# Kernel tuning notes

Measured on AMD Instinct MI355X. Metric: run time of the kernel, lower is better.

The kernel has to match this reference:

```python
import jax, jax.numpy as jnp
import numpy as np
import math

B_SZ = 2
SEQ = 4000
D_MODEL = 768
D_INNER = 1536
D_STATE = 16
D_CONV = 4
DT_RANK = 48
NSLICES = 5


def setup_inputs() -> dict:
    key = jax.random.key(0)
    ks = jax.random.split(key, 9)
    s = 0.02
    hidden_states = jax.random.normal(ks[0], (B_SZ, SEQ, D_MODEL), jnp.float32)
    in_proj_w = jax.random.normal(ks[1], (2 * D_INNER, D_MODEL), jnp.float32) * s
    conv_w = jax.random.normal(ks[2], (3, D_INNER, 1, D_CONV), jnp.float32) * 0.3
    x_proj_w = jax.random.normal(ks[3], (3, DT_RANK + 2 * D_STATE, D_INNER), jnp.float32) * s
    dt_proj_w = jax.random.uniform(ks[4], (3, D_INNER, DT_RANK), jnp.float32,
                                   -(DT_RANK ** -0.5), DT_RANK ** -0.5)
    # dt bias: inverse-softplus of dt ~ LogUniform(1e-3, 0.1), as in the torch init
    dt = jnp.exp(jax.random.uniform(ks[5], (3, D_INNER), jnp.float32)
                 * (math.log(0.1) - math.log(1e-3)) + math.log(1e-3))
    dt = jnp.clip(dt, 1e-4, None)
    dt_bias = dt + jnp.log(-jnp.expm1(-dt))
    A = jnp.broadcast_to(jnp.arange(1, D_STATE + 1, dtype=jnp.float32), (D_INNER, D_STATE))
    A_log = jnp.broadcast_to(jnp.log(A), (3, D_INNER, D_STATE))
    D_param = jnp.ones((3, D_INNER), jnp.float32)
    out_proj_w = jax.random.normal(ks[6], (D_MODEL, D_INNER), jnp.float32) * s
    return dict(hidden_states=hidden_states, in_proj_w=in_proj_w, conv_w=conv_w,
                x_proj_w=x_proj_w, dt_proj_w=dt_proj_w, dt_bias=dt_bias,
                A_log=A_log, D_param=D_param, out_proj_w=out_proj_w)


def _mamba_branch(xz, cw, xpw, dpw, db, A_log, Dv):
    # xz: [B, 2*d_inner, L]. Equivalent of mamba_inner_fn_no_out_proj.
    x, z = jnp.split(xz, 2, axis=1)                      # [B, d, L] each
    # depthwise causal conv1d (left pad d_conv-1, output length L)
    xc = jax.lax.conv_general_dilated(
        x, cw, window_strides=(1,), padding=[(D_CONV - 1, 0)],
        feature_group_count=D_INNER,
        dimension_numbers=('NCH', 'OIH', 'NCH'))
    x = jax.nn.silu(xc)
    x_dbl = jnp.einsum('bdl,ed->bel', x, xpw)            # [B, dt_rank+2n, L]
    dtr, Bm, Cm = jnp.split(x_dbl, [DT_RANK, DT_RANK + D_STATE], axis=1)
    delta = jax.nn.softplus(jnp.einsum('brl,dr->bdl', dtr, dpw) + db[None, :, None])
    A = -jnp.exp(A_log)                                  # [d, n]

    def step(h, inp):
        d_t, x_t, B_t, C_t = inp                         # [B,d],[B,d],[B,n],[B,n]
        h = h * jnp.exp(d_t[..., None] * A) + (d_t * x_t)[..., None] * B_t[:, None, :]
        y = jnp.einsum('bdn,bn->bd', h, C_t)
        return h, y

    inputs = (jnp.moveaxis(delta, 2, 0), jnp.moveaxis(x, 2, 0),
              jnp.moveaxis(Bm, 2, 0), jnp.moveaxis(Cm, 2, 0))
    h0 = jnp.zeros((x.shape[0], D_INNER, D_STATE), x.dtype)
    _, ys = jax.lax.scan(step, h0, inputs)               # ys: [L, B, d]
    y = jnp.moveaxis(ys, 0, 2)                           # [B, d, L]
    y = y + Dv[None, :, None] * x
    return y * jax.nn.silu(z)


def reference(hidden_states, in_proj_w, conv_w, x_proj_w, dt_proj_w, dt_bias,
              A_log, D_param, out_proj_w):
    b, l, _ = hidden_states.shape
    lc = l // NSLICES
    xz = jnp.einsum('bld,ed->bel', hidden_states, in_proj_w)   # [B, 2d, L]
    # branch 0: forward
    out0 = _mamba_branch(xz, conv_w[0], x_proj_w[0], dt_proj_w[0], dt_bias[0],
                         A_log[0], D_param[0])
    # branch 1: reversed sequence
    out1 = _mamba_branch(xz[:, :, ::-1], conv_w[1], x_proj_w[1], dt_proj_w[1],
                         dt_bias[1], A_log[1], D_param[1])[:, :, ::-1]
    # branch 2: slice-interleaved (chunk into nslices, stack, flatten)
    xz2 = xz.reshape(b, 2 * D_INNER, NSLICES, lc).transpose(0, 1, 3, 2).reshape(b, 2 * D_INNER, l)
    out2 = _mamba_branch(xz2, conv_w[2], x_proj_w[2], dt_proj_w[2], dt_bias[2],
                         A_log[2], D_param[2])
    out2 = out2.reshape(b, D_INNER, lc, NSLICES).transpose(0, 1, 3, 2).reshape(b, D_INNER, l)
    out = out0 + out1 + out2
    return jnp.einsum('bdl,od->blo', out, out_proj_w)          # [B, L, d_model]
```

## Files before the change

kernel.cpp:

```cpp
#include <hip/hip_runtime.h>
#include <math.h>

#define L_SEQ 4000
#define DM 768
#define DI 1536
#define DS 16
#define DTRK 48
#define NCH 50
#define LC 80
#define NBL 8000

typedef __attribute__((ext_vector_type(8))) short short8;
typedef __attribute__((ext_vector_type(8))) unsigned short ushort8;
typedef __attribute__((ext_vector_type(4))) unsigned short ushort4v;
typedef __attribute__((ext_vector_type(4))) float floatx4;
typedef __attribute__((ext_vector_type(2))) float float2v;

__device__ __forceinline__ float silu_f(float x) { return x / (1.f + __expf(-x)); }
__device__ __forceinline__ float softplus_f(float x) {
  return fmaxf(x, 0.f) + __logf(1.f + __expf(-fabsf(x)));
}
__device__ __forceinline__ int map_t(int branch, int t) {
  if (branch == 0) return t;
  if (branch == 1) return L_SEQ - 1 - t;
  return (t % 5) * 800 + t / 5;
}
__device__ __forceinline__ unsigned short f2bf(float f) {
  unsigned int u = __float_as_uint(f);
  u = (u + 0x7fffu + ((u >> 16) & 1u)) >> 16;
  return (unsigned short)u;
}
__device__ __forceinline__ float bf2f(unsigned short u) {
  return __uint_as_float(((unsigned int)u) << 16);
}
__device__ __forceinline__ void glds16(const void* g, void* l) {
  __builtin_amdgcn_global_load_lds((const __attribute__((address_space(1))) void*)g,
                                   (__attribute__((address_space(3))) void*)l, 16, 0, 0);
}
__device__ __forceinline__ void pow_ladder2(float E1, float2v* dc2) {
  float E2 = E1 * E1;
  float E4 = E2 * E2;
  float E8 = E4 * E4;
  float2v v4 = {E4, E4}, v8 = {E8, E8};
  dc2[0] = (float2v){E1, E2};
  dc2[1] = dc2[0] * (float2v){E2, E2};
  dc2[2] = dc2[0] * v4;
  dc2[3] = dc2[1] * v4;
  dc2[4] = dc2[0] * v8;
  dc2[5] = dc2[1] * v8;
  dc2[6] = dc2[2] * v8;
  dc2[7] = dc2[3] * v8;
}

__device__ __forceinline__ void cast_seg(const float* __restrict__ src,
                                         unsigned short* __restrict__ dst,
                                         int blk, int n) {
  int i = (blk * 256 + (int)threadIdx.x) * 8;
  if (i >= n) return;
  float4 v0 = *(const float4*)&src[i];
  float4 v1 = *(const float4*)&src[i + 4];
  ushort8 r;
  r[0] = f2bf(v0.x); r[1] = f2bf(v0.y); r[2] = f2bf(v0.z); r[3] = f2bf(v0.w);
  r[4] = f2bf(v1.x); r[5] = f2bf(v1.y); r[6] = f2bf(v1.z); r[7] = f2bf(v1.w);
  *(ushort8*)&dst[i] = r;
}
__global__ __launch_bounds__(256) void k_cast5(const float* s0, unsigned short* d0,
                                               const float* s1, unsigned short* d1,
                                               const float* s2, unsigned short* d2,
                                               const float* s3, unsigned short* d3,
                                               const float* s4, unsigned short* d4) {
  int blk = blockIdx.x;
  if (blk < 3000)      cast_seg(s0, d0, blk,        6144000);
  else if (blk < 4152) cast_seg(s1, d1, blk - 3000, 2359296);
  else if (blk < 4728) cast_seg(s2, d2, blk - 4152, 1179648);
  else if (blk < 4836) cast_seg(s3, d3, blk - 4728, 221184);
  else                 cast_seg(s4, d4, blk - 4836, 368640);
}

template <int KDIM, int KA, int MODE, int MT, int NBLK>
__global__ __launch_bounds__(256) void k_gemm_bt(const unsigned short* __restrict__ A,
                                                 const unsigned short* __restrict__ B,
                                                 float* __restrict__ O0f,
                                                 unsigned short* __restrict__ O0h,
                                                 unsigned short* __restrict__ O1h) {
  __shared__ unsigned short As[128 * 32];
  __shared__ unsigned short Bs[128 * 32];
  constexpr int Q = NBLK / 8, R = NBLK % 8;
  int xcd = blockIdx.x & 7;
  int slot = blockIdx.x >> 3;
  int start = xcd * Q + (xcd < R ? xcd : R);
  int j = start + slot;
  int m0 = (j % MT) * 128;
  int n0 = (j / MT) * 128;
  int tid = threadIdx.x;
  int lane = tid & 63;
  int wm = (tid >> 6) & 1;
  int wn = tid >> 7;
  int srow = tid >> 2;
  int skof = (tid & 3) * 8;
  int brow0 = n0 + srow;       if (brow0 >= NBL) brow0 = NBL - 1;
  int brow1 = n0 + srow + 64;  if (brow1 >= NBL) brow1 = NBL - 1;
  floatx4 zero = {0.f, 0.f, 0.f, 0.f};
  floatx4 acc[4][4];
#pragma unroll
  for (int i = 0; i < 4; ++i)
#pragma unroll
    for (int j2 = 0; j2 < 4; ++j2) acc[i][j2] = zero;
  int ar = wm * 64 + (lane & 15);
  int br = wn * 64 + (lane & 15);
  int kq = (lane >> 4) * 8;
  for (int k0 = 0; k0 < KDIM; k0 += 32) {
    int ka = (k0 % KA);
    glds16(&A[(size_t)(m0 + srow) * KA + ka + skof],      &As[tid * 8]);
    glds16(&A[(size_t)(m0 + srow + 64) * KA + ka + skof], &As[tid * 8 + 2048]);
    glds16(&B[(size_t)brow0 * KDIM + k0 + skof], &Bs[tid * 8]);
    glds16(&B[(size_t)brow1 * KDIM + k0 + skof], &Bs[tid * 8 + 2048]);
    __syncthreads();
    short8 a[4], b[4];
#pragma unroll
    for (int i = 0; i < 4; ++i) a[i] = *(const short8*)&As[(ar + i * 16) * 32 + kq];
#pragma unroll
    for (int i = 0; i < 4; ++i) b[i] = *(const short8*)&Bs[(br + i * 16) * 32 + kq];
#pragma unroll
    for (int mt = 0; mt < 4; ++mt)
#pragma unroll
      for (int nt = 0; nt < 4; ++nt)
        acc[mt][nt] = __builtin_amdgcn_mfma_f32_16x16x32_bf16(a[mt], b[nt], acc[mt][nt], 0, 0, 0);
    __syncthreads();
  }
  int mq = m0 + wm * 64 + ((lane >> 4) << 2);
  int nq = n0 + wn * 64 + (lane & 15);
#pragma unroll
  for (int nt = 0; nt < 4; ++nt) {
    int n = nq + nt * 16;
    if (n >= NBL) continue;
#pragma unroll
    for (int mt = 0; mt < 4; ++mt) {
      int m = mq + mt * 16;
      floatx4 v = acc[mt][nt];
      if (MODE == 0) {
        *(floatx4*)&O0f[(size_t)n * DM + m] = v;
      } else {
        if (m < DI) {
          ushort4v r;
          r[0] = f2bf(v[0]); r[1] = f2bf(v[1]); r[2] = f2bf(v[2]); r[3] = f2bf(v[3]);
          *(ushort4v*)&O0h[(size_t)n * DI + m] = r;
        } else {
          ushort4v r;
          r[0] = f2bf(silu_f(v[0])); r[1] = f2bf(silu_f(v[1]));
          r[2] = f2bf(silu_f(v[2])); r[3] = f2bf(silu_f(v[3]));
          *(ushort4v*)&O1h[(size_t)n * DI + m - DI] = r;
        }
      }
    }
  }
}

__global__ __launch_bounds__(256) void k_conv_all(const unsigned short* __restrict__ xTB,
                                                  const float* __restrict__ cw_all,
                                                  unsigned short* __restrict__ xaB) {
  int z = blockIdx.z;
  int brn = z >> 1, b = z & 1;
  int d = blockIdx.x * 256 + threadIdx.x;
  int t0 = blockIdx.y * 8;
  const unsigned short* xrow = xTB + (size_t)b * L_SEQ * DI;
  float4 w = *(const float4*)&cw_all[((size_t)brn * DI + d) * 4];
  float xm3 = (t0 >= 3) ? bf2f(xrow[(size_t)map_t(brn, t0 - 3) * DI + d]) : 0.f;
  float xm2 = (t0 >= 2) ? bf2f(xrow[(size_t)map_t(brn, t0 - 2) * DI + d]) : 0.f;
  float xm1 = (t0 >= 1) ? bf2f(xrow[(size_t)map_t(brn, t0 - 1) * DI + d]) : 0.f;
#pragma unroll
  for (int i = 0; i < 8; ++i) {
    int t = t0 + i;
    float xc = bf2f(xrow[(size_t)map_t(brn, t) * DI + d]);
    float xa = silu_f(fmaf(w.w, xc, fmaf(w.z, xm1, fmaf(w.y, xm2, w.x * xm3))));
    xaB[((size_t)z * L_SEQ + t) * DI + d] = f2bf(xa);
    xm3 = xm2; xm2 = xm1; xm1 = xc;
  }
}

__global__ __launch_bounds__(256) void k_xprojm(const unsigned short* __restrict__ xpwB,
                                                const unsigned short* __restrict__ xaB,
                                                unsigned short* __restrict__ dtrB,
                                                float* __restrict__ BC) {
  __shared__ unsigned short As[128 * 32];
  __shared__ unsigned short Bs[128 * 32];
  int z = blockIdx.z;
  int brn = z >> 1;
  int n0 = blockIdx.x * 128;
  int tid = threadIdx.x;
  int lane = tid & 63;
  int wm = (tid >> 6) & 1;
  int wn = tid >> 7;
  int srow = tid >> 2;
  int skof = (tid & 3) * 8;
  int arow0 = srow;       if (arow0 > 79) arow0 = 79;
  int arow1 = srow + 64;  if (arow1 > 79) arow1 = 79;
  int brow0 = n0 + srow;       if (brow0 >= L_SEQ) brow0 = L_SEQ - 1;
  int brow1 = n0 + srow + 64;  if (brow1 >= L_SEQ) brow1 = L_SEQ - 1;
  const unsigned short* A = xpwB + (size_t)brn * 80 * DI;
  const unsigned short* Bm = xaB + (size_t)z * L_SEQ * DI;
  floatx4 zero = {0.f, 0.f, 0.f, 0.f};
  floatx4 acc[4][4];
#pragma unroll
  for (int i = 0; i < 4; ++i)
#pragma unroll
    for (int j = 0; j < 4; ++j) acc[i][j] = zero;
  int ar = wm * 64 + (lane & 15);
  int br = wn * 64 + (lane & 15);
  int kq = (lane >> 4) * 8;
  for (int k0 = 0; k0 < DI; k0 += 32) {
    glds16(&A[(size_t)arow0 * DI + k0 + skof], &As[tid * 8]);
    glds16(&A[(size_t)arow1 * DI + k0 + skof], &As[tid * 8 + 2048]);
    glds16(&Bm[(size_t)brow0 * DI + k0 + skof], &Bs[tid * 8]);
    glds16(&Bm[(size_t)brow1 * DI + k0 + skof], &Bs[tid * 8 + 2048]);
    __syncthreads();
    short8 a[4], b[4];
#pragma unroll
    for (int i = 0; i < 4; ++i) a[i] = *(const short8*)&As[(ar + i * 16) * 32 + kq];
#pragma unroll
    for (int i = 0; i < 4; ++i) b[i] = *(const short8*)&Bs[(br + i * 16) * 32 + kq];
#pragma unroll
    for (int mt = 0; mt < 4; ++mt)
#pragma unroll
      for (int nt = 0; nt < 4; ++nt)
        acc[mt][nt] = __builtin_amdgcn_mfma_f32_16x16x32_bf16(a[mt], b[nt], acc[mt][nt], 0, 0, 0);
    __syncthreads();
  }
  int mq = wm * 64 + ((lane >> 4) << 2);
  int nq = n0 + wn * 64 + (lane & 15);
#pragma unroll
  for (int nt = 0; nt < 4; ++nt) {
    int t = nq + nt * 16;
    if (t >= L_SEQ) continue;
#pragma unroll
    for (int mt = 0; mt < 4; ++mt) {
      int j = mq + mt * 16;
      if (j >= 80) continue;
      floatx4 v = acc[mt][nt];
      if (j < 48) {
        ushort4v r;
        r[0] = f2bf(v[0]); r[1] = f2bf(v[1]); r[2] = f2bf(v[2]); r[3] = f2bf(v[3]);
        *(ushort4v*)&dtrB[((size_t)z * L_SEQ + t) * DTRK + j] = r;
      } else {
#pragma unroll
        for (int r = 0; r < 4; ++r)
          BC[((size_t)z * 32 + (j + r - 48)) * L_SEQ + t] = v[r];
      }
    }
  }
}

__global__ __launch_bounds__(256) void k_dtg(const unsigned short* __restrict__ dpwB,
                                             const unsigned short* __restrict__ dtrB,
                                             const float* __restrict__ dbias,
                                             unsigned short* __restrict__ dT) {
  __shared__ unsigned short As[128 * 64];
  __shared__ unsigned short Bs[128 * 64];
  int z = blockIdx.z;
  int brn = z >> 1;
  int m0 = blockIdx.y * 128;
  int n0 = blockIdx.x * 128;
  int tid = threadIdx.x;
  int lane = tid & 63;
  int wm = (tid >> 6) & 1;
  int wn = tid >> 7;
  {
    int zr = tid >> 1, zs = 6 + (tid & 1);
    ushort8 zz = {0, 0, 0, 0, 0, 0, 0, 0};
    *(ushort8*)&As[zr * 64 + ((zs ^ (zr & 7)) << 3)] = zz;
    *(ushort8*)&Bs[zr * 64 + ((zs ^ (zr & 7)) << 3)] = zz;
  }
  {
    int row = tid >> 1;
    int p0 = (tid & 1) * 3;
    const unsigned short* Ag = dpwB + (size_t)brn * DI * DTRK + (size_t)(m0 + row) * DTRK;
    int bro = n0 + row; if (bro > L_SEQ - 1) bro = L_SEQ - 1;
    const unsigned short* Bg = dtrB + ((size_t)z * L_SEQ + bro) * DTRK;
#pragma unroll
    for (int i = 0; i < 3; ++i) {
      int slot = p0 + i;
      int off = (slot ^ (row & 7)) << 3;
      *(ushort8*)&As[row * 64 + off] = *(const ushort8*)&Ag[slot << 3];
      *(ushort8*)&Bs[row * 64 + off] = *(const ushort8*)&Bg[slot << 3];
    }
  }
  __syncthreads();
  int ar = wm * 64 + (lane & 15);
  int brr = wn * 64 + (lane & 15);
  int kslot = lane >> 4;
  floatx4 zero = {0.f, 0.f, 0.f, 0.f};
  floatx4 acc[4][4];
#pragma unroll
  for (int i = 0; i < 4; ++i)
#pragma unroll
    for (int j = 0; j < 4; ++j) acc[i][j] = zero;
#pragma unroll
  for (int kk = 0; kk < 2; ++kk) {
    short8 a[4], b[4];
    int slot = kk * 4 + kslot;
#pragma unroll
    for (int i = 0; i < 4; ++i) {
      int r = ar + i * 16;
      a[i] = *(const short8*)&As[r * 64 + ((slot ^ (r & 7)) << 3)];
    }
#pragma unroll
    for (int i = 0; i < 4; ++i) {
      int r = brr + i * 16;
      b[i] = *(const short8*)&Bs[r * 64 + ((slot ^ (r & 7)) << 3)];
    }
#pragma unroll
    for (int mt = 0; mt < 4; ++mt)
#pragma unroll
      for (int nt = 0; nt < 4; ++nt)
        acc[mt][nt] = __builtin_amdgcn_mfma_f32_16x16x32_bf16(a[mt], b[nt], acc[mt][nt], 0, 0, 0);
  }
  int mq = m0 + wm * 64 + ((lane >> 4) << 2);
  int nq = n0 + wn * 64 + (lane & 15);
  float4 bi[4];
#pragma unroll
  for (int mt = 0; mt < 4; ++mt)
    bi[mt] = *(const float4*)&dbias[(size_t)brn * DI + mq + mt * 16];
#pragma unroll
  for (int nt = 0; nt < 4; ++nt) {
    int n = nq + nt * 16;
    if (n >= L_SEQ) continue;
#pragma unroll
    for (int mt = 0; mt < 4; ++mt) {
      int m = mq + mt * 16;
      floatx4 v = acc[mt][nt];
      ushort4v r;
      r[0] = f2bf(softplus_f(v[0] + bi[mt].x));
      r[1] = f2bf(softplus_f(v[1] + bi[mt].y));
      r[2] = f2bf(softplus_f(v[2] + bi[mt].z));
      r[3] = f2bf(softplus_f(v[3] + bi[mt].w));
      *(ushort4v*)&dT[((size_t)z * L_SEQ + n) * DI + m] = r;
    }
  }
}

__device__ __forceinline__ void load_a2(const float* __restrict__ A_log, int brn, int d,
                                        float* a2, bool& fastp) {
  fastp = true;
#pragma unroll
  for (int g = 0; g < 4; ++g) {
    float4 v = *(const float4*)&A_log[((size_t)brn * DI + d) * DS + g * 4];
    float av0 = __expf(v.x), av1 = __expf(v.y), av2 = __expf(v.z), av3 = __expf(v.w);
    a2[g * 4 + 0] = -av0 * 1.44269504f; a2[g * 4 + 1] = -av1 * 1.44269504f;
    a2[g * 4 + 2] = -av2 * 1.44269504f; a2[g * 4 + 3] = -av3 * 1.44269504f;
    fastp = fastp && fabsf(av0 - (float)(g * 4 + 1)) < 1e-3f
                  && fabsf(av1 - (float)(g * 4 + 2)) < 1e-3f
                  && fabsf(av2 - (float)(g * 4 + 3)) < 1e-3f
                  && fabsf(av3 - (float)(g * 4 + 4)) < 1e-3f;
  }
}

#define S1_BODY(T, XV, DLV)                                                       \
  do {                                                                            \
    S += (DLV);                                                                   \
    float dtx_ = (DLV) * (XV);                                                    \
    float2v dc2[8];                                                               \
    if (fastp) {                                                                  \
      pow_ladder2(exp2f(-(DLV) * 1.44269504f), dc2);                              \
    } else {                                                                      \
      _Pragma("unroll")                                                           \
      for (int i = 0; i < 8; ++i)                                                 \
        dc2[i] = (float2v){exp2f((DLV) * a2[2 * i]), exp2f((DLV) * a2[2 * i + 1])}; \
    }                                                                             \
    const float2v* B2 = (const float2v*)&BtS[(T)][0];                             \
    float2v dtx2 = {dtx_, dtx_};                                                  \
    _Pragma("unroll")                                                             \
    for (int i = 0; i < 8; ++i)                                                   \
      h2[i] = __builtin_elementwise_fma(h2[i], dc2[i], dtx2 * B2[i]);             \
  } while (0)

__global__ __launch_bounds__(256) void k_scan1c(const unsigned short* __restrict__ xaB,
                                                const unsigned short* __restrict__ dT,
                                                const float* __restrict__ BC,
                                                const float* __restrict__ A_log,
                                                float* __restrict__ hO,
                                                float* __restrict__ Sc) {
  __shared__ float BtS[LC][16];
  int z = blockIdx.z;
  int brn = z >> 1;
  int ch = blockIdx.y;
  int t0 = ch * LC;
  int d = blockIdx.x * 256 + threadIdx.x;
  int tid = threadIdx.x;
  for (int i = tid; i < 320; i += 256) {
    int row = i / 20;
    int c4 = (i % 20) * 4;
    float4 v = *(const float4*)&BC[((size_t)z * 32 + row) * L_SEQ + t0 + c4];
    BtS[c4 + 0][row] = v.x; BtS[c4 + 1][row] = v.y;
    BtS[c4 + 2][row] = v.z; BtS[c4 + 3][row] = v.w;
  }
  float a2[16]; bool fastp;
  load_a2(A_log, brn, d, a2, fastp);
  const unsigned short* xbp = xaB + ((size_t)z * L_SEQ + t0) * DI + d;
  const unsigned short* dbp = dT + ((size_t)z * L_SEQ + t0) * DI + d;
  float2v h2[8];
#pragma unroll
  for (int i = 0; i < 8; ++i) h2[i] = (float2v){0.f, 0.f};
  float S = 0.f;
  unsigned short rx_a = xbp[0],      rd_a = dbp[0];
  unsigned short rx_b = xbp[DI],     rd_b = dbp[DI];
  unsigned short rx_c = xbp[2 * DI], rd_c = dbp[2 * DI];
  unsigned short rx_d = xbp[3 * DI], rd_d = dbp[3 * DI];
  __syncthreads();
  for (int t4 = 0; t4 < LC; t4 += 4) {
    { float xv = bf2f(rx_a), dv = bf2f(rd_a); S1_BODY(t4 + 0, xv, dv); }
    { int tc = (t4 + 4 < LC) ? t4 + 4 : LC - 1; rx_a = xbp[tc * DI]; rd_a = dbp[tc * DI]; }
    { float xv = bf2f(rx_b), dv = bf2f(rd_b); S1_BODY(t4 + 1, xv, dv); }
    { int tc = (t4 + 5 < LC) ? t4 + 5 : LC - 1; rx_b = xbp[tc * DI]; rd_b = dbp[tc * DI]; }
    { float xv = bf2f(rx_c), dv = bf2f(rd_c); S1_BODY(t4 + 2, xv, dv); }
    { int tc = (t4 + 6 < LC) ? t4 + 6 : LC - 1; rx_c = xbp[tc * DI]; rd_c = dbp[tc * DI]; }
    { float xv = bf2f(rx_d), dv = bf2f(rd_d); S1_BODY(t4 + 3, xv, dv); }
    { int tc = (t4 + 7 < LC) ? t4 + 7 : LC - 1; rx_d = xbp[tc * DI]; rd_d = dbp[tc * DI]; }
  }
  size_t base = (((size_t)z * NCH + ch) * DI + d) * 16;
#pragma unroll
  for (int i = 0; i < 8; ++i) *(float2v*)&hO[base + i * 2] = h2[i];
  Sc[((size_t)z * NCH + ch) * DI + d] = S;
}

__global__ __launch_bounds__(256) void k_scan2c(float* __restrict__ hO,
                                                const float* __restrict__ Sc,
                                                const float* __restrict__ A_log) {
  int idx = blockIdx.x * 256 + threadIdx.x;
  int z = idx / (DI * 16);
  int rem = idx % (DI * 16);
  int brn = z >> 1;
  float a2 = -__expf(A_log[(size_t)brn * DI * DS + rem]) * 1.44269504f;
  const int HS = DI * 16;
  size_t p = (size_t)z * NCH * HS + rem;
  size_t q = (size_t)z * NCH * DI + (rem >> 4);
  float th_a = hO[p];            float s_a = Sc[q];
  float th_b = hO[p + HS];       float s_b = Sc[q + DI];
  float th_c = hO[p + 2 * HS];   float s_c = Sc[q + 2 * DI];
  float th_d = hO[p + 3 * HS];   float s_d = Sc[q + 3 * DI];
  float H = 0.f;
  for (int c4 = 0; c4 < 48; c4 += 4) {
    hO[p] = H; H = fmaf(exp2f(s_a * a2), H, th_a);
    th_a = hO[p + 4 * HS]; s_a = Sc[q + 4 * DI];
    p += HS; q += DI;
    hO[p] = H; H = fmaf(exp2f(s_b * a2), H, th_b);
    th_b = hO[p + 4 * HS]; s_b = Sc[q + 4 * DI];
    p += HS; q += DI;
    hO[p] = H; H = fmaf(exp2f(s_c * a2), H, th_c);
    if (c4 + 6 < NCH) { th_c = hO[p + 4 * HS]; s_c = Sc[q + 4 * DI]; }
    p += HS; q += DI;
    hO[p] = H; H = fmaf(exp2f(s_d * a2), H, th_d);
    if (c4 + 7 < NCH) { th_d = hO[p + 4 * HS]; s_d = Sc[q + 4 * DI]; }
    p += HS; q += DI;
  }
  hO[p] = H; H = fmaf(exp2f(s_a * a2), H, th_a); p += HS;
  hO[p] = H;
}

template <int BRN>
__global__ __launch_bounds__(256) void k_scan3x(const unsigned short* __restrict__ xaB,
                                                const unsigned short* __restrict__ dT,
                                                const float* __restrict__ BC,
                                                const float* __restrict__ A_log,
                                                const float* __restrict__ Dp,
                                                const float* __restrict__ hO,
                                                const unsigned short* __restrict__ szTB,
                                                unsigned short* __restrict__ ybuf) {
  __shared__ float BCt[LC][32];
  int b = blockIdx.z;
  int z = BRN * 2 + b;
  int ch = blockIdx.y;
  int t0 = ch * LC;
  int d = blockIdx.x * 256 + threadIdx.x;
  int tid = threadIdx.x;
  for (int i = tid; i < 640; i += 256) {
    int row = i / 20;
    int c4 = (i % 20) * 4;
    float4 v = *(const float4*)&BC[((size_t)z * 32 + row) * L_SEQ + t0 + c4];
    BCt[c4 + 0][row] = v.x; BCt[c4 + 1][row] = v.y;
    BCt[c4 + 2][row] = v.z; BCt[c4 + 3][row] = v.w;
  }
  float a2[16]; bool fastp;
  load_a2(A_log, BRN, d, a2, fastp);
  float Dv = Dp[(size_t)BRN * DI + d];
  float2v h2[8];
  size_t hbase = (((size_t)z * NCH + ch) * DI + d) * 16;
#pragma unroll
  for (int i = 0; i < 8; ++i) h2[i] = *(const float2v*)&hO[hbase + i * 2];
  int mt = map_t(BRN, t0);
  const unsigned short* pxa = xaB + ((size_t)z * L_SEQ + t0) * DI + d;
  const unsigned short* pdl = dT + ((size_t)z * L_SEQ + t0) * DI + d;
  const unsigned short* psz = szTB + ((size_t)b * L_SEQ + mt) * DI + d;
  unsigned short* pyb = ybuf + ((size_t)b * L_SEQ + mt) * (3 * DI) + BRN * DI + d;
  int p5 = t0 % 5;
  __syncthreads();
  float xa = bf2f(*pxa);
  float del = bf2f(*pdl);
  float sz = bf2f(*psz);
  for (int t = 0; t < LC - 1; ++t) {
    int stepS;
    if (BRN == 0) stepS = DI;
    else if (BRN == 1) stepS = -DI;
    else {
      ++p5;
      if (p5 == 5) { p5 = 0; stepS = -3199 * DI; }
      else stepS = 800 * DI;
    }
    float xan = bf2f(pxa[DI]);
    float deln = bf2f(pdl[DI]);
    float szn;
    if (BRN == 0) szn = bf2f(psz[DI]);
    else if (BRN == 1) szn = bf2f(psz[-DI]);
    else szn = bf2f(psz[stepS]);
    float dtx = del * xa;
    float2v dc2[8];
    if (fastp) {
      pow_ladder2(exp2f(-del * 1.44269504f), dc2);
    } else {
#pragma unroll
      for (int i = 0; i < 8; ++i)
        dc2[i] = (float2v){exp2f(del * a2[2 * i]), exp2f(del * a2[2 * i + 1])};
    }
    const float2v* B2 = (const float2v*)&BCt[t][0];
    const float2v* C2 = (const float2v*)&BCt[t][16];
    float2v dtx2 = {dtx, dtx};
    float2v y2a = {0.f, 0.f}, y2b = {0.f, 0.f};
#pragma unroll
    for (int i = 0; i < 4; ++i) {
      h2[i] = __builtin_elementwise_fma(h2[i], dc2[i], dtx2 * B2[i]);
      y2a = __builtin_elementwise_fma(h2[i], C2[i], y2a);
    }
#pragma unroll
    for (int i = 4; i < 8; ++i) {
      h2[i] = __builtin_elementwise_fma(h2[i], dc2[i], dtx2 * B2[i]);
      y2b = __builtin_elementwise_fma(h2[i], C2[i], y2b);
    }
    float y = (y2a[0] + y2a[1]) + (y2b[0] + y2b[1]) + Dv * xa;
    *pyb = f2bf(y * sz);
    pxa += DI; pdl += DI; psz += stepS; pyb += stepS * 3;
    xa = xan; del = deln; sz = szn;
  }
  {
    float dtx = del * xa;
    float2v dc2[8];
    if (fastp) {
      pow_ladder2(exp2f(-del * 1.44269504f), dc2);
    } else {
#pragma unroll
      for (int i = 0; i < 8; ++i)
        dc2[i] = (float2v){exp2f(del * a2[2 * i]), exp2f(del * a2[2 * i + 1])};
    }
    const float2v* B2 = (const float2v*)&BCt[LC - 1][0];
    const float2v* C2 = (const float2v*)&BCt[LC - 1][16];
    float2v dtx2 = {dtx, dtx};
    float2v y2a = {0.f, 0.f}, y2b = {0.f, 0.f};
#pragma unroll
    for (int i = 0; i < 4; ++i) {
      h2[i] = __builtin_elementwise_fma(h2[i], dc2[i], dtx2 * B2[i]);
      y2a = __builtin_elementwise_fma(h2[i], C2[i], y2a);
    }
#pragma unroll
    for (int i = 4; i < 8; ++i) {
      h2[i] = __builtin_elementwise_fma(h2[i], dc2[i], dtx2 * B2[i]);
      y2b = __builtin_elementwise_fma(h2[i], C2[i], y2b);
    }
    float y = (y2a[0] + y2a[1]) + (y2b[0] + y2b[1]) + Dv * xa;
    *pyb = f2bf(y * sz);
  }
}

#define S3B(T, XV, DLV, SZV, MS)                                                  \
  do {                                                                            \
    float xa_ = silu_f(fmaf(w.w, (XV), fmaf(w.z, xm1, fmaf(w.y, xm2, w.x * xm3)))); \
    float dtx_ = (DLV) * xa_;                                                     \
    float2v dc2[8];                                                               \
    if (fastp) {                                                                  \
      pow_ladder2(exp2f(-(DLV) * 1.44269504f), dc2);                              \
    } else {                                                                      \
      _Pragma("unroll")                                                           \
      for (int i = 0; i < 8; ++i)                                                 \
        dc2[i] = (float2v){exp2f((DLV) * a2[2 * i]), exp2f((DLV) * a2[2 * i + 1])}; \
    }                                                                             \
    const float2v* B2 = (const float2v*)&BCt[(T)][0];                             \
    const float2v* C2 = (const float2v*)&BCt[(T)][16];                            \
    float2v dtx2 = {dtx_, dtx_};                                                  \
    float2v y2a = {0.f, 0.f}, y2b = {0.f, 0.f};                                   \
    _Pragma("unroll")                                                             \
    for (int i = 0; i < 4; ++i) {                                                 \
      h2[i] = __builtin_elementwise_fma(h2[i], dc2[i], dtx2 * B2[i]);             \
      y2a = __builtin_elementwise_fma(h2[i], C2[i], y2a);                         \
    }                                                                             \
    _Pragma("unroll")                                                             \
    for (int i = 4; i < 8; ++i) {                                                 \
      h2[i] = __builtin_elementwise_fma(h2[i], dc2[i], dtx2 * B2[i]);             \
      y2b = __builtin_elementwise_fma(h2[i], C2[i], y2b);                         \
    }                                                                             \
    float y_ = (y2a[0] + y2a[1]) + (y2b[0] + y2b[1]) + Dv * xa_;                  \
    yb[(size_t)(MS) * (3 * DI)] = f2bf(y_ * (SZV));                               \
    xm3 = xm2; xm2 = xm1; xm1 = (XV);                                             \
  } while (0)

__global__ __launch_bounds__(256) void k_scan3c(const unsigned short* __restrict__ xTB,
                                                const unsigned short* __restrict__ dT,
                                                const float* __restrict__ BC,
                                                const float* __restrict__ cw_all,
                                                const float* __restrict__ A_log,
                                                const float* __restrict__ Dp,
                                                const float* __restrict__ hO,
                                                const unsigned short* __restrict__ szTB,
                                                unsigned short* __restrict__ ybuf) {
  __shared__ float BCt[LC][32];
  int z = blockIdx.z;
  int brn = z >> 1, b = z & 1;
  int ch = blockIdx.y;
  int t0 = ch * LC;
  int d = blockIdx.x * 256 + threadIdx.x;
  int tid = threadIdx.x;
  for (int i = tid; i < 640; i += 256) {
    int row = i / 20;
    int c4 = (i % 20) * 4;
    float4 v = *(const float4*)&BC[((size_t)z * 32 + row) * L_SEQ + t0 + c4];
    BCt[c4 + 0][row] = v.x; BCt[c4 + 1][row] = v.y;
    BCt[c4 + 2][row] = v.z; BCt[c4 + 3][row] = v.w;
  }
  float4 w = *(const float4*)&cw_all[((size_t)brn * DI + d) * 4];
  float a2[16]; bool fastp;
  load_a2(A_log, brn, d, a2, fastp);
  float Dv = Dp[(size_t)brn * DI + d];
  const unsigned short* xb  = xTB + (size_t)b * L_SEQ * DI + d;
  const unsigned short* db  = dT + ((size_t)z * L_SEQ + t0) * DI + d;
  const unsigned short* szb = szTB + (size_t)b * L_SEQ * DI + d;
  unsigned short* yb = ybuf + (size_t)b * L_SEQ * (3 * DI) + (size_t)brn * DI + d;
  float2v h2[8];
  size_t hbase = (((size_t)z * NCH + ch) * DI + d) * 16;
#pragma unroll
  for (int i = 0; i < 8; ++i) h2[i] = *(const float2v*)&hO[hbase + i * 2];
  bool isb2 = (brn == 2);
  int mbase = (brn == 1) ? (L_SEQ - 1 - t0) : t0;
  int msign = (brn == 1) ? -1 : 1;
  int chb = ch * 16;
  auto mrow = [&](int tt) -> int {
    if (isb2) return (tt % 5) * 800 + chb + tt / 5;
    return mbase + msign * tt;
  };
  float xm3 = (t0 >= 3) ? bf2f(xb[(size_t)map_t(brn, t0 - 3) * DI]) : 0.f;
  float xm2 = (t0 >= 2) ? bf2f(xb[(size_t)map_t(brn, t0 - 2) * DI]) : 0.f;
  float xm1 = (t0 >= 1) ? bf2f(xb[(size_t)map_t(brn, t0 - 1) * DI]) : 0.f;
  int my_a = mrow(0), my_b = mrow(1), my_c = mrow(2), my_d = mrow(3);
  unsigned short rx_a = xb[(size_t)my_a * DI], rs_a = szb[(size_t)my_a * DI], rl_a = db[0];
  unsigned short rx_b = xb[(size_t)my_b * DI], rs_b = szb[(size_t)my_b * DI], rl_b = db[DI];
  unsigned short rx_c = xb[(size_t)my_c * DI], rs_c = szb[(size_t)my_c * DI], rl_c = db[2 * DI];
  unsigned short rx_d = xb[(size_t)my_d * DI], rs_d = szb[(size_t)my_d * DI], rl_d = db[3 * DI];
  __syncthreads();
  for (int t4 = 0; t4 < LC; t4 += 4) {
    { float xv = bf2f(rx_a), dv = bf2f(rl_a), sv = bf2f(rs_a);
      S3B(t4 + 0, xv, dv, sv, my_a); }
    { int tc = (t4 + 4 < LC) ? t4 + 4 : LC - 1; my_a = mrow(tc);
      rx_a = xb[(size_t)my_a * DI]; rs_a = szb[(size_t)my_a * DI]; rl_a = db[tc * DI]; }
    { float xv = bf2f(rx_b), dv = bf2f(rl_b), sv = bf2f(rs_b);
      S3B(t4 + 1, xv, dv, sv, my_b); }
    { int tc = (t4 + 5 < LC) ? t4 + 5 : LC - 1; my_b = mrow(tc);
      rx_b = xb[(size_t)my_b * DI]; rs_b = szb[(size_t)my_b * DI]; rl_b = db[tc * DI]; }
    { float xv = bf2f(rx_c), dv = bf2f(rl_c), sv = bf2f(rs_c);
      S3B(t4 + 2, xv, dv, sv, my_c); }
    { int tc = (t4 + 6 < LC) ? t4 + 6 : LC - 1; my_c = mrow(tc);
      rx_c = xb[(size_t)my_c * DI]; rs_c = szb[(size_t)my_c * DI]; rl_c = db[tc * DI]; }
    { float xv = bf2f(rx_d), dv = bf2f(rl_d), sv = bf2f(rs_d);
      S3B(t4 + 3, xv, dv, sv, my_d); }
    { int tc = (t4 + 7 < LC) ? t4 + 7 : LC - 1; my_d = mrow(tc);
      rx_d = xb[(size_t)my_d * DI]; rs_d = szb[(size_t)my_d * DI]; rl_d = db[tc * DI]; }
  }
}

extern "C" void kernel_launch(void* const* d_in, const int* in_sizes, int n_in,
                              void* d_out, int out_size, void* d_ws, size_t ws_size,
                              hipStream_t stream) {
  const float* hs        = (const float*)d_in[0];
  const float* in_proj_w = (const float*)d_in[1];
  const float* conv_w    = (const float*)d_in[2];
  const float* x_proj_w  = (const float*)d_in[3];
  const float* dt_proj_w = (const float*)d_in[4];
  const float* dt_bias   = (const float*)d_in[5];
  const float* A_log     = (const float*)d_in[6];
  const float* D_param   = (const float*)d_in[7];
  const float* out_proj_w= (const float*)d_in[8];
  float* out = (float*)d_out;
  float* ws = (float*)d_ws;

  unsigned short* xTB  = (unsigned short*)(ws);
  unsigned short* szTB = (unsigned short*)(ws + 6144000);
  unsigned short* dtrB = (unsigned short*)(ws + 12288000);
  float* BC            = ws + 12864000;
  unsigned short* dT   = (unsigned short*)(ws + 13632000);
  float* hO            = ws + 32064000;
  float* Sc            = ws + 39436800;
  unsigned short* dpwB = (unsigned short*)(ws + 39897600);
  unsigned short* OWb  = (unsigned short*)(ws + 40008192);
  unsigned short* hsB  = (unsigned short*)(ws + 40598016);
  unsigned short* Wb   = hsB + 6144000;
  unsigned short* xaB  = (unsigned short*)(ws + 40598016);
  unsigned short* xpwB = (unsigned short*)(ws + 59030016);
  unsigned short* ybufBig = (unsigned short*)(ws + 59214336);
  bool big = ws_size >= (size_t)77646336 * 4;
  unsigned short* ybuf = big ? ybufBig : xaB;

  k_cast5<<<5016, 256, 0, stream>>>(hs, hsB, in_proj_w, Wb, out_proj_w, OWb,
                                    dt_proj_w, dpwB, x_proj_w, xpwB);

  k_gemm_bt<DM, DM, 1, 24, 1512><<<1512, 256, 0, stream>>>(Wb, hsB, nullptr, xTB, szTB);

  k_conv_all<<<dim3(6, 500, 6), 256, 0, stream>>>(xTB, conv_w, xaB);
  k_xprojm<<<dim3(32, 1, 6), 256, 0, stream>>>(xpwB, xaB, dtrB, BC);
  k_dtg<<<dim3(32, 12, 6), 256, 0, stream>>>(dpwB, dtrB, dt_bias, dT);

  k_scan1c<<<dim3(6, NCH, 6), 256, 0, stream>>>(xaB, dT, BC, A_log, hO, Sc);
  k_scan2c<<<576, 256, 0, stream>>>(hO, Sc, A_log);
  if (big) {
    k_scan3x<0><<<dim3(6, NCH, 2), 256, 0, stream>>>(xaB, dT, BC, A_log, D_param, hO, szTB, ybuf);
    k_scan3x<1><<<dim3(6, NCH, 2), 256, 0, stream>>>(xaB, dT, BC, A_log, D_param, hO, szTB, ybuf);
    k_scan3x<2><<<dim3(6, NCH, 2), 256, 0, stream>>>(xaB, dT, BC, A_log, D_param, hO, szTB, ybuf);
  } else {
    k_scan3c<<<dim3(6, NCH, 6), 256, 0, stream>>>(xTB, dT, BC, conv_w, A_log, D_param,
                                                  hO, szTB, ybuf);
  }

  k_gemm_bt<3 * DI, DI, 0, 6, 378><<<378, 256, 0, stream>>>(OWb, ybuf, out, nullptr, nullptr);
}
```

Before: 557.1 us.

## Write scan outputs in place over delta and gather branch rows in out-proj GEMM

The three per-branch scan3x launches are replaced by one k_scan3d launch that writes y*silu(z) in branch-major, scan-time order into the dT buffer, overwriting the delta values already consumed. The out-projection GEMM gains a BMAJ mode that computes per-row base offsets for each branch's time permutation (forward, reversed, slice-interleaved). It then gathers B tiles directly from that buffer instead of a separate token-major ybuf. This removes the extra ybuf workspace, the scattered interleaved writes, and the three separate launches. The cost is non-contiguous B loads in the GEMM, where rows map to different time indices per branch.

```diff
diff --git a/kernel.cpp b/kernel.cpp
--- a/kernel.cpp
+++ b/kernel.cpp
@@ -77,7 +77,7 @@
   else                 cast_seg(s4, d4, blk - 4836, 368640);
 }
 
-template <int KDIM, int KA, int MODE, int MT, int NBLK>
+template <int KDIM, int KA, int MODE, int MT, int NBLK, int BMAJ = 0>
 __global__ __launch_bounds__(256) void k_gemm_bt(const unsigned short* __restrict__ A,
                                                  const unsigned short* __restrict__ B,
                                                  float* __restrict__ O0f,
@@ -100,6 +100,20 @@
   int skof = (tid & 3) * 8;
   int brow0 = n0 + srow;       if (brow0 >= NBL) brow0 = NBL - 1;
   int brow1 = n0 + srow + 64;  if (brow1 >= NBL) brow1 = NBL - 1;
+  size_t rb0a = 0, rb0b = 0, rb0c = 0, rb1a = 0, rb1b = 0, rb1c = 0;
+  if (BMAJ) {
+    int bb0 = brow0 >= L_SEQ ? 1 : 0, l0 = brow0 - bb0 * L_SEQ;
+    int bb1 = brow1 >= L_SEQ ? 1 : 0, l1 = brow1 - bb1 * L_SEQ;
+    int t1_0 = L_SEQ - 1 - l0, t1_1 = L_SEQ - 1 - l1;
+    int t2_0 = 5 * (l0 % 800) + l0 / 800;
+    int t2_1 = 5 * (l1 % 800) + l1 / 800;
+    rb0a = ((size_t)(0 + bb0) * L_SEQ + l0) * DI;
+    rb0b = ((size_t)(2 + bb0) * L_SEQ + t1_0) * DI;
+    rb0c = ((size_t)(4 + bb0) * L_SEQ + t2_0) * DI;
+    rb1a = ((size_t)(0 + bb1) * L_SEQ + l1) * DI;
+    rb1b = ((size_t)(2 + bb1) * L_SEQ + t1_1) * DI;
+    rb1c = ((size_t)(4 + bb1) * L_SEQ + t2_1) * DI;
+  }
   floatx4 zero = {0.f, 0.f, 0.f, 0.f};
   floatx4 acc[4][4];
 #pragma unroll
@@ -109,12 +123,22 @@
   int ar = wm * 64 + (lane & 15);
   int br = wn * 64 + (lane & 15);
   int kq = (lane >> 4) * 8;
+  int brnk = 0, dd0 = 0;
   for (int k0 = 0; k0 < KDIM; k0 += 32) {
     int ka = (k0 % KA);
     glds16(&A[(size_t)(m0 + srow) * KA + ka + skof],      &As[tid * 8]);
     glds16(&A[(size_t)(m0 + srow + 64) * KA + ka + skof], &As[tid * 8 + 2048]);
-    glds16(&B[(size_t)brow0 * KDIM + k0 + skof], &Bs[tid * 8]);
-    glds16(&B[(size_t)brow1 * KDIM + k0 + skof], &Bs[tid * 8 + 2048]);
+    if (BMAJ) {
+      size_t b0 = brnk == 0 ? rb0a : (brnk == 1 ? rb0b : rb0c);
+      size_t b1 = brnk == 0 ? rb1a : (brnk == 1 ? rb1b : rb1c);
+      glds16(&B[b0 + dd0 + skof], &Bs[tid * 8]);
+      glds16(&B[b1 + dd0 + skof], &Bs[tid * 8 + 2048]);
+      dd0 += 32;
+      if (dd0 == DI) { dd0 = 0; ++brnk; }
+    } else {
+      glds16(&B[(size_t)brow0 * KDIM + k0 + skof], &Bs[tid * 8]);
+      glds16(&B[(size_t)brow1 * KDIM + k0 + skof], &Bs[tid * 8 + 2048]);
+    }
     __syncthreads();
     short8 a[4], b[4];
 #pragma unroll
@@ -456,122 +480,9 @@
   hO[p] = H;
 }
 
-template <int BRN>
-__global__ __launch_bounds__(256) void k_scan3x(const unsigned short* __restrict__ xaB,
-                                                const unsigned short* __restrict__ dT,
-                                                const float* __restrict__ BC,
-                                                const float* __restrict__ A_log,
-                                                const float* __restrict__ Dp,
-                                                const float* __restrict__ hO,
-                                                const unsigned short* __restrict__ szTB,
-                                                unsigned short* __restrict__ ybuf) {
-  __shared__ float BCt[LC][32];
-  int b = blockIdx.z;
-  int z = BRN * 2 + b;
-  int ch = blockIdx.y;
-  int t0 = ch * LC;
-  int d = blockIdx.x * 256 + threadIdx.x;
-  int tid = threadIdx.x;
-  for (int i = tid; i < 640; i += 256) {
-    int row = i / 20;
-    int c4 = (i % 20) * 4;
-    float4 v = *(const float4*)&BC[((size_t)z * 32 + row) * L_SEQ + t0 + c4];
-    BCt[c4 + 0][row] = v.x; BCt[c4 + 1][row] = v.y;
-    BCt[c4 + 2][row] = v.z; BCt[c4 + 3][row] = v.w;
-  }
-  float a2[16]; bool fastp;
-  load_a2(A_log, BRN, d, a2, fastp);
-  float Dv = Dp[(size_t)BRN * DI + d];
-  float2v h2[8];
-  size_t hbase = (((size_t)z * NCH + ch) * DI + d) * 16;
-#pragma unroll
-  for (int i = 0; i < 8; ++i) h2[i] = *(const float2v*)&hO[hbase + i * 2];
-  int mt = map_t(BRN, t0);
-  const unsigned short* pxa = xaB + ((size_t)z * L_SEQ + t0) * DI + d;
-  const unsigned short* pdl = dT + ((size_t)z * L_SEQ + t0) * DI + d;
-  const unsigned short* psz = szTB + ((size_t)b * L_SEQ + mt) * DI + d;
-  unsigned short* pyb = ybuf + ((size_t)b * L_SEQ + mt) * (3 * DI) + BRN * DI + d;
-  int p5 = t0 % 5;
-  __syncthreads();
-  float xa = bf2f(*pxa);
-  float del = bf2f(*pdl);
-  float sz = bf2f(*psz);
-  for (int t = 0; t < LC - 1; ++t) {
-    int stepS;
-    if (BRN == 0) stepS = DI;
-    else if (BRN == 1) stepS = -DI;
-    else {
-      ++p5;
-      if (p5 == 5) { p5 = 0; stepS = -3199 * DI; }
-      else stepS = 800 * DI;
-    }
-    float xan = bf2f(pxa[DI]);
-    float deln = bf2f(pdl[DI]);
-    float szn;
-    if (BRN == 0) szn = bf2f(psz[DI]);
-    else if (BRN == 1) szn = bf2f(psz[-DI]);
-    else szn = bf2f(psz[stepS]);
-    float dtx = del * xa;
-    float2v dc2[8];
-    if (fastp) {
-      pow_ladder2(exp2f(-del * 1.44269504f), dc2);
-    } else {
-#pragma unroll
-      for (int i = 0; i < 8; ++i)
-        dc2[i] = (float2v){exp2f(del * a2[2 * i]), exp2f(del * a2[2 * i + 1])};
-    }
-    const float2v* B2 = (const float2v*)&BCt[t][0];
-    const float2v* C2 = (const float2v*)&BCt[t][16];
-    float2v dtx2 = {dtx, dtx};
-    float2v y2a = {0.f, 0.f}, y2b = {0.f, 0.f};
-#pragma unroll
-    for (int i = 0; i < 4; ++i) {
-      h2[i] = __builtin_elementwise_fma(h2[i], dc2[i], dtx2 * B2[i]);
-      y2a = __builtin_elementwise_fma(h2[i], C2[i], y2a);
-    }
-#pragma unroll
-    for (int i = 4; i < 8; ++i) {
-      h2[i] = __builtin_elementwise_fma(h2[i], dc2[i], dtx2 * B2[i]);
-      y2b = __builtin_elementwise_fma(h2[i], C2[i], y2b);
-    }
-    float y = (y2a[0] + y2a[1]) + (y2b[0] + y2b[1]) + Dv * xa;
-    *pyb = f2bf(y * sz);
-    pxa += DI; pdl += DI; psz += stepS; pyb += stepS * 3;
-    xa = xan; del = deln; sz = szn;
-  }
-  {
-    float dtx = del * xa;
-    float2v dc2[8];
-    if (fastp) {
-      pow_ladder2(exp2f(-del * 1.44269504f), dc2);
-    } else {
-#pragma unroll
-      for (int i = 0; i < 8; ++i)
-        dc2[i] = (float2v){exp2f(del * a2[2 * i]), exp2f(del * a2[2 * i + 1])};
-    }
-    const float2v* B2 = (const float2v*)&BCt[LC - 1][0];
-    const float2v* C2 = (const float2v*)&BCt[LC - 1][16];
-    float2v dtx2 = {dtx, dtx};
-    float2v y2a = {0.f, 0.f}, y2b = {0.f, 0.f};
-#pragma unroll
-    for (int i = 0; i < 4; ++i) {
-      h2[i] = __builtin_elementwise_fma(h2[i], dc2[i], dtx2 * B2[i]);
-      y2a = __builtin_elementwise_fma(h2[i], C2[i], y2a);
-    }
-#pragma unroll
-    for (int i = 4; i < 8; ++i) {
-      h2[i] = __builtin_elementwise_fma(h2[i], dc2[i], dtx2 * B2[i]);
-      y2b = __builtin_elementwise_fma(h2[i], C2[i], y2b);
-    }
-    float y = (y2a[0] + y2a[1]) + (y2b[0] + y2b[1]) + Dv * xa;
-    *pyb = f2bf(y * sz);
-  }
-}
-
-#define S3B(T, XV, DLV, SZV, MS)                                                  \
+#define S3D(T, XV, DLV, SZV)                                                      \
   do {                                                                            \
-    float xa_ = silu_f(fmaf(w.w, (XV), fmaf(w.z, xm1, fmaf(w.y, xm2, w.x * xm3)))); \
-    float dtx_ = (DLV) * xa_;                                                     \
+    float dtx_ = (DLV) * (XV);                                                    \
     float2v dc2[8];                                                               \
     if (fastp) {                                                                  \
       pow_ladder2(exp2f(-(DLV) * 1.44269504f), dc2);                              \
@@ -594,20 +505,17 @@
       h2[i] = __builtin_elementwise_fma(h2[i], dc2[i], dtx2 * B2[i]);             \
       y2b = __builtin_elementwise_fma(h2[i], C2[i], y2b);                         \
     }                                                                             \
-    float y_ = (y2a[0] + y2a[1]) + (y2b[0] + y2b[1]) + Dv * xa_;                  \
-    yb[(size_t)(MS) * (3 * DI)] = f2bf(y_ * (SZV));                               \
-    xm3 = xm2; xm2 = xm1; xm1 = (XV);                                             \
+    float y_ = (y2a[0] + y2a[1]) + (y2b[0] + y2b[1]) + Dv * (XV);                 \
+    dp[(size_t)(T) * DI] = f2bf(y_ * (SZV));                                      \
   } while (0)
 
-__global__ __launch_bounds__(256) void k_scan3c(const unsigned short* __restrict__ xTB,
-                                                const unsigned short* __restrict__ dT,
+__global__ __launch_bounds__(256) void k_scan3d(const unsigned short* __restrict__ xaB,
+                                                unsigned short* __restrict__ dT,
                                                 const float* __restrict__ BC,
-                                                const float* __restrict__ cw_all,
                                                 const float* __restrict__ A_log,
                                                 const float* __restrict__ Dp,
                                                 const float* __restrict__ hO,
-                                                const unsigned short* __restrict__ szTB,
-                                                unsigned short* __restrict__ ybuf) {
+                                                const unsigned short* __restrict__ szTB) {
   __shared__ float BCt[LC][32];
   int z = blockIdx.z;
   int brn = z >> 1, b = z & 1;
@@ -622,14 +530,12 @@
     BCt[c4 + 0][row] = v.x; BCt[c4 + 1][row] = v.y;
     BCt[c4 + 2][row] = v.z; BCt[c4 + 3][row] = v.w;
   }
-  float4 w = *(const float4*)&cw_all[((size_t)brn * DI + d) * 4];
   float a2[16]; bool fastp;
   load_a2(A_log, brn, d, a2, fastp);
   float Dv = Dp[(size_t)brn * DI + d];
-  const unsigned short* xb  = xTB + (size_t)b * L_SEQ * DI + d;
-  const unsigned short* db  = dT + ((size_t)z * L_SEQ + t0) * DI + d;
+  const unsigned short* xp = xaB + ((size_t)z * L_SEQ + t0) * DI + d;
+  unsigned short* dp = dT + ((size_t)z * L_SEQ + t0) * DI + d;
   const unsigned short* szb = szTB + (size_t)b * L_SEQ * DI + d;
-  unsigned short* yb = ybuf + (size_t)b * L_SEQ * (3 * DI) + (size_t)brn * DI + d;
   float2v h2[8];
   size_t hbase = (((size_t)z * NCH + ch) * DI + d) * 16;
 #pragma unroll
@@ -642,32 +548,24 @@
     if (isb2) return (tt % 5) * 800 + chb + tt / 5;
     return mbase + msign * tt;
   };
-  float xm3 = (t0 >= 3) ? bf2f(xb[(size_t)map_t(brn, t0 - 3) * DI]) : 0.f;
-  float xm2 = (t0 >= 2) ? bf2f(xb[(size_t)map_t(brn, t0 - 2) * DI]) : 0.f;
-  float xm1 = (t0 >= 1) ? bf2f(xb[(size_t)map_t(brn, t0 - 1) * DI]) : 0.f;
-  int my_a = mrow(0), my_b = mrow(1), my_c = mrow(2), my_d = mrow(3);
-  unsigned short rx_a = xb[(size_t)my_a * DI], rs_a = szb[(size_t)my_a * DI], rl_a = db[0];
-  unsigned short rx_b = xb[(size_t)my_b * DI], rs_b = szb[(size_t)my_b * DI], rl_b = db[DI];
-  unsigned short rx_c = xb[(size_t)my_c * DI], rs_c = szb[(size_t)my_c * DI], rl_c = db[2 * DI];
-  unsigned short rx_d = xb[(size_t)my_d * DI], rs_d = szb[(size_t)my_d * DI], rl_d = db[3 * DI];
+  unsigned short rx_a = xp[0],      rl_a = dp[0],      rs_a = szb[(size_t)mrow(0) * DI];
+  unsigned short rx_b = xp[DI],     rl_b = dp[DI],     rs_b = szb[(size_t)mrow(1) * DI];
+  unsigned short rx_c = xp[2 * DI], rl_c = dp[2 * DI], rs_c = szb[(size_t)mrow(2) * DI];
+  unsigned short rx_d = xp[3 * DI], rl_d = dp[3 * DI], rs_d = szb[(size_t)mrow(3) * DI];
   __syncthreads();
   for (int t4 = 0; t4 < LC; t4 += 4) {
-    { float xv = bf2f(rx_a), dv = bf2f(rl_a), sv = bf2f(rs_a);
-      S3B(t4 + 0, xv, dv, sv, my_a); }
-    { int tc = (t4 + 4 < LC) ? t4 + 4 : LC - 1; my_a = mrow(tc);
-      rx_a = xb[(size_t)my_a * DI]; rs_a = szb[(size_t)my_a * DI]; rl_a = db[tc * DI]; }
-    { float xv = bf2f(rx_b), dv = bf2f(rl_b), sv = bf2f(rs_b);
-      S3B(t4 + 1, xv, dv, sv, my_b); }
-    { int tc = (t4 + 5 < LC) ? t4 + 5 : LC - 1; my_b = mrow(tc);
-      rx_b = xb[(size_t)my_b * DI]; rs_b = szb[(size_t)my_b * DI]; rl_b = db[tc * DI]; }
-    { float xv = bf2f(rx_c), dv = bf2f(rl_c), sv = bf2f(rs_c);
-      S3B(t4 + 2, xv, dv, sv, my_c); }
-    { int tc = (t4 + 6 < LC) ? t4 + 6 : LC - 1; my_c = mrow(tc);
-      rx_c = xb[(size_t)my_c * DI]; rs_c = szb[(size_t)my_c * DI]; rl_c = db[tc * DI]; }
-    { float xv = bf2f(rx_d), dv = bf2f(rl_d), sv = bf2f(rs_d);
-      S3B(t4 + 3, xv, dv, sv, my_d); }
-    { int tc = (t4 + 7 < LC) ? t4 + 7 : LC - 1; my_d = mrow(tc);
-      rx_d = xb[(size_t)my_d * DI]; rs_d = szb[(size_t)my_d * DI]; rl_d = db[tc * DI]; }
+    { float xv = bf2f(rx_a), dv = bf2f(rl_a), sv = bf2f(rs_a); S3D(t4 + 0, xv, dv, sv); }
+    { int tc = (t4 + 4 < LC) ? t4 + 4 : LC - 1;
+      rx_a = xp[(size_t)tc * DI]; rl_a = dp[(size_t)tc * DI]; rs_a = szb[(size_t)mrow(tc) * DI]; }
+    { float xv = bf2f(rx_b), dv = bf2f(rl_b), sv = bf2f(rs_b); S3D(t4 + 1, xv, dv, sv); }
+    { int tc = (t4 + 5 < LC) ? t4 + 5 : LC - 1;
+      rx_b = xp[(size_t)tc * DI]; rl_b = dp[(size_t)tc * DI]; rs_b = szb[(size_t)mrow(tc) * DI]; }
+    { float xv = bf2f(rx_c), dv = bf2f(rl_c), sv = bf2f(rs_c); S3D(t4 + 2, xv, dv, sv); }
+    { int tc = (t4 + 6 < LC) ? t4 + 6 : LC - 1;
+      rx_c = xp[(size_t)tc * DI]; rl_c = dp[(size_t)tc * DI]; rs_c = szb[(size_t)mrow(tc) * DI]; }
+    { float xv = bf2f(rx_d), dv = bf2f(rl_d), sv = bf2f(rs_d); S3D(t4 + 3, xv, dv, sv); }
+    { int tc = (t4 + 7 < LC) ? t4 + 7 : LC - 1;
+      rx_d = xp[(size_t)tc * DI]; rl_d = dp[(size_t)tc * DI]; rs_d = szb[(size_t)mrow(tc) * DI]; }
   }
 }
 
@@ -699,9 +597,6 @@
   unsigned short* Wb   = hsB + 6144000;
   unsigned short* xaB  = (unsigned short*)(ws + 40598016);
   unsigned short* xpwB = (unsigned short*)(ws + 59030016);
-  unsigned short* ybufBig = (unsigned short*)(ws + 59214336);
-  bool big = ws_size >= (size_t)77646336 * 4;
-  unsigned short* ybuf = big ? ybufBig : xaB;
 
   k_cast5<<<5016, 256, 0, stream>>>(hs, hsB, in_proj_w, Wb, out_proj_w, OWb,
                                     dt_proj_w, dpwB, x_proj_w, xpwB);
@@ -714,14 +609,7 @@
 
   k_scan1c<<<dim3(6, NCH, 6), 256, 0, stream>>>(xaB, dT, BC, A_log, hO, Sc);
   k_scan2c<<<576, 256, 0, stream>>>(hO, Sc, A_log);
-  if (big) {
-    k_scan3x<0><<<dim3(6, NCH, 2), 256, 0, stream>>>(xaB, dT, BC, A_log, D_param, hO, szTB, ybuf);
-    k_scan3x<1><<<dim3(6, NCH, 2), 256, 0, stream>>>(xaB, dT, BC, A_log, D_param, hO, szTB, ybuf);
-    k_scan3x<2><<<dim3(6, NCH, 2), 256, 0, stream>>>(xaB, dT, BC, A_log, D_param, hO, szTB, ybuf);
-  } else {
-    k_scan3c<<<dim3(6, NCH, 6), 256, 0, stream>>>(xTB, dT, BC, conv_w, A_log, D_param,
-                                                  hO, szTB, ybuf);
-  }
-
-  k_gemm_bt<3 * DI, DI, 0, 6, 378><<<378, 256, 0, stream>>>(OWb, ybuf, out, nullptr, nullptr);
-}
+  k_scan3d<<<dim3(6, NCH, 6), 256, 0, stream>>>(xaB, dT, BC, A_log, D_param, hO, szTB);
+
+  k_gemm_bt<3 * DI, DI, 0, 6, 378, 1><<<378, 256, 0, stream>>>(OWb, dT, out, nullptr, nullptr);
+}
```

Result: no change. 563.6 us (+1.2%).
